# Kernel tuning notes

Hardware: AMD Instinct MI355X
Metric: run time of the kernel (lower is better)

The kernel has to match this reference:

```python
import jax, jax.numpy as jnp
import numpy as np

N_NODES = 50000
N_EDGES = 250000
D = 300
ATOM_VOCAB = 5001   # len(atom_map) + 1
WORD_VOCAB = 30000
N_GRAPHS = 1000
NUM_HOPS = 4


def setup_inputs() -> dict:
    key = jax.random.key(0)
    ks = jax.random.split(key, 6)
    x = jax.random.randint(ks[0], (N_NODES, 2), 0, 5000)            # (atom_id, word_id) per node
    edge_index = jax.random.randint(ks[1], (2, N_EDGES), 0, N_NODES)
    batch = jnp.sort(jax.random.randint(ks[2], (N_NODES,), 0, N_GRAPHS))
    atom_table = jax.random.normal(ks[3], (ATOM_VOCAB, D), dtype=jnp.float32) * 0.02
    word_table = jax.random.normal(ks[4], (WORD_VOCAB, D), dtype=jnp.float32) * 0.02
    W = jax.random.normal(ks[5], (D, D), dtype=jnp.float32) / jnp.sqrt(jnp.float32(D))
    b = jnp.zeros((D,), dtype=jnp.float32)
    return {"x": x, "edge_index": edge_index, "batch": batch, "num_hops": NUM_HOPS,
            "atom_table": atom_table, "word_table": word_table, "W": W, "b": b}


def reference(x, edge_index, batch, num_hops, atom_table, word_table, W, b):
    N = x.shape[0]
    # node embedding: atom + word lookup
    h = atom_table[x[:, 0]] + word_table[x[:, 1]]                    # [N, D]

    # GCN normalization with self-loops (PyG GCNConv defaults)
    loops = jnp.arange(N)
    src = jnp.concatenate([edge_index[0], loops])                    # [E+N]
    dst = jnp.concatenate([edge_index[1], loops])                    # [E+N]
    deg = jax.ops.segment_sum(jnp.ones_like(src, dtype=h.dtype), dst, num_segments=N)
    dinv = jax.lax.rsqrt(jnp.where(deg > 0, deg, 1.0))
    norm = dinv[src] * dinv[dst]                                     # [E+N]

    for _ in range(num_hops):
        hl = h @ W                                                   # [N, D] linear transform
        msg = hl[src] * norm[:, None]                                # gather + normalize
        h = jax.ops.segment_sum(msg, dst, num_segments=N) + b        # scatter-add + bias

    # global mean pool over graphs
    sums = jax.ops.segment_sum(h, batch, num_segments=N_GRAPHS)      # [G, D]
    counts = jax.ops.segment_sum(jnp.ones((N,), h.dtype), batch, num_segments=N_GRAPHS)
    return sums / jnp.clip(counts, 1.0)[:, None]
```

## Files before the change

kernel.cpp:

```cpp
#include <hip/hip_runtime.h>
#include <hip/hip_fp16.h>

#define D    300
#define DC   75
#define SCB  1024
#define PGRP 6

typedef _Float16 half4v __attribute__((ext_vector_type(4)));

__global__ __launch_bounds__(256) void embed_f16(const int* __restrict__ x,
                                                 const float4* __restrict__ atomT,
                                                 const float4* __restrict__ wordT,
                                                 half4v* __restrict__ h, int N) {
    int idx = blockIdx.x * blockDim.x + threadIdx.x;
    if (idx >= N * DC) return;
    int n = idx / DC, c = idx - n * DC;
    int a = x[n * 2 + 0];
    int w = x[n * 2 + 1];
    float4 va = atomT[(size_t)a * DC + c];
    float4 vw = wordT[(size_t)w * DC + c];
    half4v o;
    o[0] = (_Float16)(va.x + vw.x);
    o[1] = (_Float16)(va.y + vw.y);
    o[2] = (_Float16)(va.z + vw.z);
    o[3] = (_Float16)(va.w + vw.w);
    h[idx] = o;
}

__global__ __launch_bounds__(256) void cnt_kernel(const int* __restrict__ dst, int* __restrict__ cnt, int E) {
    int i = blockIdx.x * blockDim.x + threadIdx.x;
    if (i < E) atomicAdd(&cnt[dst[i]], 1);
}
__global__ __launch_bounds__(SCB) void scan1_kernel(const int* __restrict__ cnt,
                                                    int* __restrict__ off, int* __restrict__ bsum,
                                                    float* __restrict__ dinv, int N) {
    __shared__ int warp_sums[16];
    const int tid = threadIdx.x;
    const int lane = tid & 63;
    const int wid = tid >> 6;
    int i = blockIdx.x * SCB + tid;
    int v = (i < N) ? cnt[i] : 0;
    if (i < N) dinv[i] = rsqrtf((float)(v + 1));
    int s = v;
    #pragma unroll
    for (int d = 1; d < 64; d <<= 1) {
        int t = __shfl_up(s, d, 64);
        if (lane >= d) s += t;
    }
    if (lane == 63) warp_sums[wid] = s;
    __syncthreads();
    if (wid == 0) {
        int ws = (lane < 16) ? warp_sums[lane] : 0;
        #pragma unroll
        for (int d = 1; d < 16; d <<= 1) {
            int t = __shfl_up(ws, d, 64);
            if (lane >= d) ws += t;
        }
        if (lane < 16) warp_sums[lane] = ws;
    }
    __syncthreads();
    int excl = (wid ? warp_sums[wid - 1] : 0) + s - v;
    if (i < N) off[i] = excl;
    if (tid == SCB - 1) bsum[blockIdx.x] = warp_sums[15];
}
__global__ __launch_bounds__(SCB) void scan2_kernel(int* __restrict__ bsum, int* __restrict__ bbase,
                                                    int* __restrict__ off, int nb, int N, int E) {
    __shared__ int warp_sums[16];
    const int tid = threadIdx.x;
    const int lane = tid & 63;
    const int wid = tid >> 6;
    int v = (tid < nb) ? bsum[tid] : 0;
    int s = v;
    #pragma unroll
    for (int d = 1; d < 64; d <<= 1) {
        int t = __shfl_up(s, d, 64);
        if (lane >= d) s += t;
    }
    if (lane == 63) warp_sums[wid] = s;
    __syncthreads();
    if (wid == 0) {
        int ws = (lane < 16) ? warp_sums[lane] : 0;
        #pragma unroll
        for (int d = 1; d < 16; d <<= 1) {
            int t = __shfl_up(ws, d, 64);
            if (lane >= d) ws += t;
        }
        if (lane < 16) warp_sums[lane] = ws;
    }
    __syncthreads();
    if (tid < nb) bbase[tid] = (wid ? warp_sums[wid - 1] : 0) + s - v;
    if (tid == 0) off[N] = E;
}
__global__ __launch_bounds__(256) void scan3_kernel(int* __restrict__ off, const int* __restrict__ bbase,
                                                    int* __restrict__ cursor, int N) {
    int i = blockIdx.x * blockDim.x + threadIdx.x;
    if (i >= N) return;
    int o = off[i] + bbase[i >> 10];
    off[i] = o;
    cursor[i] = o;
}
__global__ __launch_bounds__(256) void fill_kernel(const int* __restrict__ src, const int* __restrict__ dst,
                                                   const float* __restrict__ dinv, int* __restrict__ cursor,
                                                   int* __restrict__ csr_src, float* __restrict__ csr_w, int E) {
    int e = blockIdx.x * blockDim.x + threadIdx.x;
    if (e >= E) return;
    int s = src[e], d = dst[e];
    int slot = atomicAdd(&cursor[d], 1);
    csr_src[slot] = s;
    csr_w[slot] = dinv[s] * dinv[d];
}
__global__ __launch_bounds__(256) void seg_start_kernel(const int* __restrict__ batch,
                                                        int* __restrict__ start, int N, int G) {
    int i = blockIdx.x * blockDim.x + threadIdx.x;
    if (i >= N) return;
    int b = batch[i];
    int prev = (i == 0) ? -1 : batch[i - 1];
    for (int g = prev + 1; g <= b; ++g) start[g] = i;
    if (i == N - 1)
        for (int g = b + 1; g <= G; ++g) start[g] = N;
}

__global__ __launch_bounds__(256) void wprep1(const float* __restrict__ W, const float* __restrict__ bias,
                                              float* __restrict__ W2, float* __restrict__ w1b) {
    int bid = blockIdx.x;
    if (bid < 352) {
        int id = bid * 256 + threadIdx.x;
        if (id >= D * D) return;
        int i = id / D, j = id % D;
        float acc = 0.f;
        #pragma unroll 4
        for (int k = 0; k < D; ++k) acc = fmaf(W[i * D + k], W[k * D + j], acc);
        W2[id] = acc;
    } else {
        int j = threadIdx.x;
        if (j >= D) return;
        float acc = 0.f;
        #pragma unroll 4
        for (int k = 0; k < D; ++k) acc = fmaf(bias[k], W[k * D + j], acc);
        w1b[j] = acc;
    }
}
__global__ __launch_bounds__(256) void wprep2(const float* __restrict__ W2, const float* __restrict__ W,
                                              const float* __restrict__ w1b,
                                              float* __restrict__ W4, float* __restrict__ w2b,
                                              float* __restrict__ w3b) {
    int bid = blockIdx.x;
    if (bid < 352) {
        int id = bid * 256 + threadIdx.x;
        if (id >= D * D) return;
        int i = id / D, j = id % D;
        float acc = 0.f;
        #pragma unroll 4
        for (int k = 0; k < D; ++k) acc = fmaf(W2[i * D + k], W2[k * D + j], acc);
        W4[id] = acc;
    } else if (bid == 352) {
        int j = threadIdx.x;
        if (j >= D) return;
        float acc = 0.f;
        #pragma unroll 4
        for (int k = 0; k < D; ++k) acc = fmaf(w1b[k], W[k * D + j], acc);
        w2b[j] = acc;
    } else {
        int j = threadIdx.x;
        if (j >= D) return;
        float acc = 0.f;
        #pragma unroll 4
        for (int k = 0; k < D; ++k) acc = fmaf(w1b[k], W2[k * D + j], acc);
        w3b[j] = acc;
    }
}

__global__ __launch_bounds__(256) void gather_f16(const half4v* __restrict__ in,
                                                  const int* __restrict__ off,
                                                  const int* __restrict__ csr_src,
                                                  const float* __restrict__ csr_w,
                                                  const float* __restrict__ dinv,
                                                  const float* __restrict__ uin,
                                                  float* __restrict__ uout,
                                                  half4v* __restrict__ out, int N) {
    int idx = blockIdx.x * blockDim.x + threadIdx.x;
    if (idx >= N * DC) return;
    int n = idx / DC, c = idx - n * DC;
    float s = dinv[n]; s = s * s;
    half4v v0 = in[idx];
    float4 acc = make_float4(s * (float)v0[0], s * (float)v0[1], s * (float)v0[2], s * (float)v0[3]);
    const bool dou = (uout != nullptr) && (c == 0);
    float uacc = 0.f;
    if (dou) uacc = s * (uin ? uin[n] : 1.0f);
    int j0 = off[n], j1 = off[n + 1];
    for (int j = j0; j < j1; ++j) {
        int sn = csr_src[j];
        float w = csr_w[j];
        half4v u = in[(size_t)sn * DC + c];
        acc.x += w * (float)u[0]; acc.y += w * (float)u[1];
        acc.z += w * (float)u[2]; acc.w += w * (float)u[3];
        if (dou) uacc += w * (uin ? uin[sn] : 1.0f);
    }
    half4v o;
    o[0] = (_Float16)acc.x; o[1] = (_Float16)acc.y;
    o[2] = (_Float16)acc.z; o[3] = (_Float16)acc.w;
    out[idx] = o;
    if (dou) uout[n] = uacc;
}

__global__ __launch_bounds__(512) void pool_final(const half4v* __restrict__ g4,
                                                  const float* __restrict__ u1,
                                                  const float* __restrict__ u2,
                                                  const float* __restrict__ u3,
                                                  const int* __restrict__ start,
                                                  const float* __restrict__ W4,
                                                  const float* __restrict__ w1b,
                                                  const float* __restrict__ w2b,
                                                  const float* __restrict__ w3b,
                                                  const float* __restrict__ bias,
                                                  float* __restrict__ out, int G) {
    __shared__ float part[PGRP][D];
    __shared__ float row[D];
    __shared__ float us[4];
    int g = blockIdx.x;
    if (g >= G) return;
    int j0 = start[g], j1 = start[g + 1];
    float inv = (j1 > j0) ? 1.0f / (float)(j1 - j0) : 0.0f;
    int tid = threadIdx.x;

    if (tid < PGRP * DC) {
        int grp = tid / DC, cc = tid - grp * DC;
        float4 acc = make_float4(0.f, 0.f, 0.f, 0.f);
        for (int n = j0 + grp; n < j1; n += PGRP) {
            half4v v = g4[(size_t)n * DC + cc];
            acc.x += (float)v[0]; acc.y += (float)v[1];
            acc.z += (float)v[2]; acc.w += (float)v[3];
        }
        part[grp][cc * 4 + 0] = acc.x;
        part[grp][cc * 4 + 1] = acc.y;
        part[grp][cc * 4 + 2] = acc.z;
        part[grp][cc * 4 + 3] = acc.w;
    } else if (tid >= 480 && tid <= 482) {
        const float* u = (tid == 480) ? u1 : (tid == 481) ? u2 : u3;
        float acc = 0.f;
        for (int n = j0; n < j1; ++n) acc += u[n];
        us[tid - 480] = acc * inv;
    } else if (tid == 483) {
        us[3] = (j1 > j0) ? 1.0f : 0.0f;
    }
    __syncthreads();
    if (tid < D) {
        float r = 0.f;
        #pragma unroll
        for (int grp = 0; grp < PGRP; ++grp) r += part[grp][tid];
        row[tid] = r * inv;
    }
    __syncthreads();

    float p1 = us[0], p2 = us[1], p3 = us[2], fl = us[3];
    if (tid < D) {
        int j = tid;
        float a0 = 0.f, a1 = 0.f, a2 = 0.f, a3 = 0.f;
        for (int k = 0; k < D; k += 4) {
            a0 = fmaf(row[k + 0], W4[(size_t)(k + 0) * D + j], a0);
            a1 = fmaf(row[k + 1], W4[(size_t)(k + 1) * D + j], a1);
            a2 = fmaf(row[k + 2], W4[(size_t)(k + 2) * D + j], a2);
            a3 = fmaf(row[k + 3], W4[(size_t)(k + 3) * D + j], a3);
        }
        float acc = (a0 + a1) + (a2 + a3);
        out[(size_t)g * D + j] = acc + p1 * w1b[j] + p2 * w2b[j] + p3 * w3b[j] + fl * bias[j];
    }
}

extern "C" void kernel_launch(void* const* d_in, const int* in_sizes, int n_in,
                              void* d_out, int out_size, void* d_ws, size_t ws_size,
                              hipStream_t stream) {
    (void)n_in; (void)ws_size;
    const int*   x     = (const int*)d_in[0];
    const int*   ei    = (const int*)d_in[1];
    const int*   batch = (const int*)d_in[2];
    const float* atomT = (const float*)d_in[4];
    const float* wordT = (const float*)d_in[5];
    const float* W     = (const float*)d_in[6];
    const float* bias  = (const float*)d_in[7];

    const int N = in_sizes[0] / 2;
    const int E = in_sizes[1] / 2;
    const int G = out_size / D;

    const int* src = ei;
    const int* dst = ei + E;

    _Float16* fA16   = (_Float16*)d_ws;
    _Float16* fB16   = fA16 + (size_t)N * D;
    float*    dinv   = (float*)(fB16 + (size_t)N * D);
    float*    csr_w  = dinv + N;
    float*    W2     = csr_w + E;
    float*    W4     = W2 + D * D;
    float*    w1b    = W4 + D * D;
    float*    w2b    = w1b + D;
    float*    w3b    = w2b + D;
    float*    u1     = w3b + D;
    float*    u2     = u1 + N;
    float*    u3     = u2 + N;
    int*      cnt    = (int*)(u3 + N);
    int*      off    = cnt + N;
    int*      cursor = off + N + 1;
    int*      csr_src= cursor + N;
    int*      bsum   = csr_src + E;
    int*      bbase  = bsum + 1024;
    int*      start  = bbase + 1024;

    const int B = 256;
    const int ndBlocks = (N * DC + B - 1) / B;
    const int nBlocks  = (N + B - 1) / B;
    const int nbScan   = (N + SCB - 1) / SCB;

    embed_f16<<<ndBlocks, B, 0, stream>>>(x, (const float4*)atomT, (const float4*)wordT, (half4v*)fA16, N);

    hipMemsetAsync(cnt, 0, (size_t)N * sizeof(int), stream);
    cnt_kernel<<<(E + B - 1) / B, B, 0, stream>>>(dst, cnt, E);
    scan1_kernel<<<nbScan, SCB, 0, stream>>>(cnt, off, bsum, dinv, N);
    scan2_kernel<<<1, SCB, 0, stream>>>(bsum, bbase, off, nbScan, N, E);
    scan3_kernel<<<nBlocks, B, 0, stream>>>(off, bbase, cursor, N);
    fill_kernel<<<(E + B - 1) / B, B, 0, stream>>>(src, dst, dinv, cursor, csr_src, csr_w, E);
    seg_start_kernel<<<nBlocks, B, 0, stream>>>(batch, start, N, G);

    wprep1<<<353, B, 0, stream>>>(W, bias, W2, w1b);
    wprep2<<<354, B, 0, stream>>>(W2, W, w1b, W4, w2b, w3b);

    gather_f16<<<ndBlocks, B, 0, stream>>>((const half4v*)fA16, off, csr_src, csr_w, dinv,
                                           nullptr, u1, (half4v*)fB16, N);
    gather_f16<<<ndBlocks, B, 0, stream>>>((const half4v*)fB16, off, csr_src, csr_w, dinv,
                                           u1, u2, (half4v*)fA16, N);
    gather_f16<<<ndBlocks, B, 0, stream>>>((const half4v*)fA16, off, csr_src, csr_w, dinv,
                                           u2, u3, (half4v*)fB16, N);
    gather_f16<<<ndBlocks, B, 0, stream>>>((const half4v*)fB16, off, csr_src, csr_w, dinv,
                                           nullptr, nullptr, (half4v*)fA16, N);

    pool_final<<<G, 512, 0, stream>>>((const half4v*)fA16, u1, u2, u3, start,
                                      W4, w1b, w2b, w3b, bias, (float*)d_out, G);
}
```

Baseline: 339.9 us.

## Fuse last propagation hop into pooling and merge setup kernels

The fourth gather pass now happens inside the pooling kernel, which aggregates neighbours per node as it accumulates each graph's sum, so the final feature buffer is never written and read back. The degree-count atomics move into the embedding kernel and the graph-start computation moves into the first scan kernel, which removes two launches. The gather kernels switch to a grid-stride loop over a fixed grid of 2048 blocks. The pooling kernel now does irregular neighbour gathers with only 1000 blocks, which may leave parallelism unused.

```diff
diff --git a/kernel.cpp b/kernel.cpp
--- a/kernel.cpp
+++ b/kernel.cpp
@@ -11,8 +11,11 @@
 __global__ __launch_bounds__(256) void embed_f16(const int* __restrict__ x,
                                                  const float4* __restrict__ atomT,
                                                  const float4* __restrict__ wordT,
-                                                 half4v* __restrict__ h, int N) {
+                                                 half4v* __restrict__ h,
+                                                 const int* __restrict__ dst, int* __restrict__ cnt,
+                                                 int E, int N) {
     int idx = blockIdx.x * blockDim.x + threadIdx.x;
+    if (idx < E) atomicAdd(&cnt[dst[idx]], 1);
     if (idx >= N * DC) return;
     int n = idx / DC, c = idx - n * DC;
     int a = x[n * 2 + 0];
@@ -27,20 +30,25 @@
     h[idx] = o;
 }
 
-__global__ __launch_bounds__(256) void cnt_kernel(const int* __restrict__ dst, int* __restrict__ cnt, int E) {
-    int i = blockIdx.x * blockDim.x + threadIdx.x;
-    if (i < E) atomicAdd(&cnt[dst[i]], 1);
-}
 __global__ __launch_bounds__(SCB) void scan1_kernel(const int* __restrict__ cnt,
                                                     int* __restrict__ off, int* __restrict__ bsum,
-                                                    float* __restrict__ dinv, int N) {
+                                                    float* __restrict__ dinv,
+                                                    const int* __restrict__ batch,
+                                                    int* __restrict__ start, int G, int N) {
     __shared__ int warp_sums[16];
     const int tid = threadIdx.x;
     const int lane = tid & 63;
     const int wid = tid >> 6;
     int i = blockIdx.x * SCB + tid;
     int v = (i < N) ? cnt[i] : 0;
-    if (i < N) dinv[i] = rsqrtf((float)(v + 1));
+    if (i < N) {
+        dinv[i] = rsqrtf((float)(v + 1));
+        int b = batch[i];
+        int prev = (i == 0) ? -1 : batch[i - 1];
+        for (int g = prev + 1; g <= b; ++g) start[g] = i;
+        if (i == N - 1)
+            for (int g = b + 1; g <= G; ++g) start[g] = N;
+    }
     int s = v;
     #pragma unroll
     for (int d = 1; d < 64; d <<= 1) {
@@ -109,16 +117,6 @@
     csr_src[slot] = s;
     csr_w[slot] = dinv[s] * dinv[d];
 }
-__global__ __launch_bounds__(256) void seg_start_kernel(const int* __restrict__ batch,
-                                                        int* __restrict__ start, int N, int G) {
-    int i = blockIdx.x * blockDim.x + threadIdx.x;
-    if (i >= N) return;
-    int b = batch[i];
-    int prev = (i == 0) ? -1 : batch[i - 1];
-    for (int g = prev + 1; g <= b; ++g) start[g] = i;
-    if (i == N - 1)
-        for (int g = b + 1; g <= G; ++g) start[g] = N;
-}
 
 __global__ __launch_bounds__(256) void wprep1(const float* __restrict__ W, const float* __restrict__ bias,
                                               float* __restrict__ W2, float* __restrict__ w1b) {
@@ -178,32 +176,37 @@
                                                   const float* __restrict__ uin,
                                                   float* __restrict__ uout,
                                                   half4v* __restrict__ out, int N) {
-    int idx = blockIdx.x * blockDim.x + threadIdx.x;
-    if (idx >= N * DC) return;
-    int n = idx / DC, c = idx - n * DC;
-    float s = dinv[n]; s = s * s;
-    half4v v0 = in[idx];
-    float4 acc = make_float4(s * (float)v0[0], s * (float)v0[1], s * (float)v0[2], s * (float)v0[3]);
-    const bool dou = (uout != nullptr) && (c == 0);
-    float uacc = 0.f;
-    if (dou) uacc = s * (uin ? uin[n] : 1.0f);
-    int j0 = off[n], j1 = off[n + 1];
-    for (int j = j0; j < j1; ++j) {
-        int sn = csr_src[j];
-        float w = csr_w[j];
-        half4v u = in[(size_t)sn * DC + c];
-        acc.x += w * (float)u[0]; acc.y += w * (float)u[1];
-        acc.z += w * (float)u[2]; acc.w += w * (float)u[3];
-        if (dou) uacc += w * (uin ? uin[sn] : 1.0f);
-    }
-    half4v o;
-    o[0] = (_Float16)acc.x; o[1] = (_Float16)acc.y;
-    o[2] = (_Float16)acc.z; o[3] = (_Float16)acc.w;
-    out[idx] = o;
-    if (dou) uout[n] = uacc;
-}
-
-__global__ __launch_bounds__(512) void pool_final(const half4v* __restrict__ g4,
+    const int stride = gridDim.x * blockDim.x;
+    for (int idx = blockIdx.x * blockDim.x + threadIdx.x; idx < N * DC; idx += stride) {
+        int n = idx / DC, c = idx - n * DC;
+        float s = dinv[n]; s = s * s;
+        half4v v0 = in[idx];
+        float4 acc = make_float4(s * (float)v0[0], s * (float)v0[1], s * (float)v0[2], s * (float)v0[3]);
+        const bool dou = (uout != nullptr) && (c == 0);
+        float uacc = 0.f;
+        if (dou) uacc = s * (uin ? uin[n] : 1.0f);
+        int j0 = off[n], j1 = off[n + 1];
+        for (int j = j0; j < j1; ++j) {
+            int sn = csr_src[j];
+            float w = csr_w[j];
+            half4v u = in[(size_t)sn * DC + c];
+            acc.x += w * (float)u[0]; acc.y += w * (float)u[1];
+            acc.z += w * (float)u[2]; acc.w += w * (float)u[3];
+            if (dou) uacc += w * (uin ? uin[sn] : 1.0f);
+        }
+        half4v o;
+        o[0] = (_Float16)acc.x; o[1] = (_Float16)acc.y;
+        o[2] = (_Float16)acc.z; o[3] = (_Float16)acc.w;
+        out[idx] = o;
+        if (dou) uout[n] = uacc;
+    }
+}
+
+__global__ __launch_bounds__(512) void pool_final(const half4v* __restrict__ g3,
+                                                  const int* __restrict__ off,
+                                                  const int* __restrict__ csr_src,
+                                                  const float* __restrict__ csr_w,
+                                                  const float* __restrict__ dinv,
                                                   const float* __restrict__ u1,
                                                   const float* __restrict__ u2,
                                                   const float* __restrict__ u3,
@@ -227,9 +230,18 @@
         int grp = tid / DC, cc = tid - grp * DC;
         float4 acc = make_float4(0.f, 0.f, 0.f, 0.f);
         for (int n = j0 + grp; n < j1; n += PGRP) {
-            half4v v = g4[(size_t)n * DC + cc];
-            acc.x += (float)v[0]; acc.y += (float)v[1];
-            acc.z += (float)v[2]; acc.w += (float)v[3];
+            float s = dinv[n]; s = s * s;
+            half4v v = g3[(size_t)n * DC + cc];
+            acc.x += s * (float)v[0]; acc.y += s * (float)v[1];
+            acc.z += s * (float)v[2]; acc.w += s * (float)v[3];
+            int e0 = off[n], e1 = off[n + 1];
+            for (int j = e0; j < e1; ++j) {
+                int sn = csr_src[j];
+                float w = csr_w[j];
+                half4v u = g3[(size_t)sn * DC + cc];
+                acc.x += w * (float)u[0]; acc.y += w * (float)u[1];
+                acc.z += w * (float)u[2]; acc.w += w * (float)u[3];
+            }
         }
         part[grp][cc * 4 + 0] = acc.x;
         part[grp][cc * 4 + 1] = acc.y;
@@ -310,29 +322,27 @@
     const int ndBlocks = (N * DC + B - 1) / B;
     const int nBlocks  = (N + B - 1) / B;
     const int nbScan   = (N + SCB - 1) / SCB;
-
-    embed_f16<<<ndBlocks, B, 0, stream>>>(x, (const float4*)atomT, (const float4*)wordT, (half4v*)fA16, N);
+    const int gatherGrid = 2048;
 
     hipMemsetAsync(cnt, 0, (size_t)N * sizeof(int), stream);
-    cnt_kernel<<<(E + B - 1) / B, B, 0, stream>>>(dst, cnt, E);
-    scan1_kernel<<<nbScan, SCB, 0, stream>>>(cnt, off, bsum, dinv, N);
+    embed_f16<<<ndBlocks, B, 0, stream>>>(x, (const float4*)atomT, (const float4*)wordT,
+                                          (half4v*)fA16, dst, cnt, E, N);
+    scan1_kernel<<<nbScan, SCB, 0, stream>>>(cnt, off, bsum, dinv, batch, start, G, N);
     scan2_kernel<<<1, SCB, 0, stream>>>(bsum, bbase, off, nbScan, N, E);
     scan3_kernel<<<nBlocks, B, 0, stream>>>(off, bbase, cursor, N);
     fill_kernel<<<(E + B - 1) / B, B, 0, stream>>>(src, dst, dinv, cursor, csr_src, csr_w, E);
-    seg_start_kernel<<<nBlocks, B, 0, stream>>>(batch, start, N, G);
 
     wprep1<<<353, B, 0, stream>>>(W, bias, W2, w1b);
     wprep2<<<354, B, 0, stream>>>(W2, W, w1b, W4, w2b, w3b);
 
-    gather_f16<<<ndBlocks, B, 0, stream>>>((const half4v*)fA16, off, csr_src, csr_w, dinv,
-                                           nullptr, u1, (half4v*)fB16, N);
-    gather_f16<<<ndBlocks, B, 0, stream>>>((const half4v*)fB16, off, csr_src, csr_w, dinv,
-                                           u1, u2, (half4v*)fA16, N);
-    gather_f16<<<ndBlocks, B, 0, stream>>>((const half4v*)fA16, off, csr_src, csr_w, dinv,
-                                           u2, u3, (half4v*)fB16, N);
-    gather_f16<<<ndBlocks, B, 0, stream>>>((const half4v*)fB16, off, csr_src, csr_w, dinv,
-                                           nullptr, nullptr, (half4v*)fA16, N);
-
-    pool_final<<<G, 512, 0, stream>>>((const half4v*)fA16, u1, u2, u3, start,
-                                      W4, w1b, w2b, w3b, bias, (float*)d_out, G);
-}
+    gather_f16<<<gatherGrid, B, 0, stream>>>((const half4v*)fA16, off, csr_src, csr_w, dinv,
+                                             nullptr, u1, (half4v*)fB16, N);
+    gather_f16<<<gatherGrid, B, 0, stream>>>((const half4v*)fB16, off, csr_src, csr_w, dinv,
+                                             u1, u2, (half4v*)fA16, N);
+    gather_f16<<<gatherGrid, B, 0, stream>>>((const half4v*)fA16, off, csr_src, csr_w, dinv,
+                                             u2, u3, (half4v*)fB16, N);
+
+    pool_final<<<G, 512, 0, stream>>>((const half4v*)fB16, off, csr_src, csr_w, dinv,
+                                      u1, u2, u3, start, W4, w1b, w2b, w3b, bias,
+                                      (float*)d_out, G);
+}
```

Result: faster. 327.8 us (-3.6%).
